# Kernel optimization log

Hardware: AMD Instinct MI355X
Metric: run time of the kernel (lower is better)

Reference implementation:

```python
import jax, jax.numpy as jnp
import numpy as np

POSE_NUM = 8192
EDGE_NUM = 1048576  # n*p = 8192*128
E = EDGE_NUM        # number of gathered edges


def setup_inputs() -> dict:
    key = jax.random.key(0)
    k1, k2, k3, k4, k5, k6 = jax.random.split(key, 6)
    # poses: [1, POSE_NUM, 7] = (tx,ty,tz, qx,qy,qz,qw) with unit quaternion (pypose SE3 convention)
    t = jax.random.normal(k1, (1, POSE_NUM, 3), jnp.float32) * 5.0
    q = jax.random.normal(k2, (1, POSE_NUM, 4), jnp.float32)
    q = q / jnp.linalg.norm(q, axis=-1, keepdims=True)
    poses = jnp.concatenate([t, q], axis=-1)
    # patch coords (r, theta): r in [1, 51], theta in [-pi, pi]
    u = jax.random.uniform(k3, (1, EDGE_NUM, 2), jnp.float32)
    r = 1.0 + 50.0 * u[..., 0:1]
    theta = (2.0 * u[..., 1:2] - 1.0) * jnp.float32(np.pi)
    patch_coords = jnp.concatenate([r, theta], axis=-1)
    # elevation angle phi: small angles typical of sonar beams
    elevation_angle = jax.random.normal(k4, (1, EDGE_NUM, 1), jnp.float32) * 0.3
    # target coords (in init_ba these come from a transform + delta; random is math-equivalent for the residual)
    target_coords = jax.random.normal(k5, (1, E, 2), jnp.float32)
    poses_idx = jax.random.randint(k6, (E,), 0, POSE_NUM, jnp.int32)
    patch_idx = jax.random.randint(jax.random.fold_in(k6, 1), (E,), 0, EDGE_NUM, jnp.int32)
    return {"poses": poses, "patch_coords": patch_coords, "elevation_angle": elevation_angle,
            "target_coords": target_coords, "poses_idx": poses_idx, "patch_idx": patch_idx}


def reference(poses, patch_coords, elevation_angle, target_coords, poses_idx, patch_idx):
    # --- gather per-edge data ---
    p = poses[0, poses_idx]                    # [E, 7]
    rt = patch_coords[0, patch_idx]            # [E, 2] (r, theta)
    phi = elevation_angle[0, patch_idx, 0]     # [E]
    r, theta = rt[:, 0], rt[:, 1]
    # --- polar -> cartesian (spherical sonar convention) ---
    cphi = jnp.cos(phi)
    pts = jnp.stack([r * cphi * jnp.cos(theta),
                     r * cphi * jnp.sin(theta),
                     r * jnp.sin(phi)], axis=-1)        # [E, 3]
    # --- SE3 action: R(q) @ pts + t, q = (qx,qy,qz,qw) unit quaternion ---
    t, qv, qw = p[:, :3], p[:, 3:6], p[:, 6:7]
    uv = jnp.cross(qv, pts)
    pts_w = pts + 2.0 * (qw * uv + jnp.cross(qv, uv)) + t  # [E, 3]
    # --- cartesian -> polar; residual only needs (r, theta) ---
    x, y, z = pts_w[:, 0], pts_w[:, 1], pts_w[:, 2]
    r_out = jnp.sqrt(x * x + y * y + z * z)
    theta_out = jnp.arctan2(y, x)
    proj = jnp.stack([r_out, theta_out], axis=-1)[None]   # [1, E, 2]
    return proj - target_coords
```

## Files before the change

### kernel.cpp

```cpp
#include <hip/hip_runtime.h>
#include <math.h>


#define EDGE_COUNT 1048576

__global__ __launch_bounds__(256) void ba_edge_kernel(
    const float*  __restrict__ poses,
    const float2* __restrict__ patch_coords,
    const float*  __restrict__ elev,
    const float2* __restrict__ target,
    const int*    __restrict__ poses_idx,
    const int*    __restrict__ patch_idx,
    float2*       __restrict__ out,
    int n)
{
    int e = blockIdx.x * blockDim.x + threadIdx.x;
    if (e >= n) return;

    const int pi = poses_idx[e];
    const int ki = patch_idx[e];

    const float2 rt  = patch_coords[ki];
    const float  phi = elev[ki];
    const float  r = rt.x, theta = rt.y;

    float sphi, cphi, st, ct;
    __sincosf(phi,   &sphi, &cphi);
    __sincosf(theta, &st,   &ct);

    const float rc = r * cphi;
    const float px = rc * ct;
    const float py = rc * st;
    const float pz = r * sphi;

    const float* p = poses + pi * 7;
    const float tx = p[0], ty = p[1], tz = p[2];
    const float qx = p[3], qy = p[4], qz = p[5], qw = p[6];

    const float ux = qy * pz - qz * py;
    const float uy = qz * px - qx * pz;
    const float uz = qx * py - qy * px;
    const float cx = qy * uz - qz * uy;
    const float cy = qz * ux - qx * uz;
    const float cz = qx * uy - qy * ux;

    const float x = px + 2.0f * (qw * ux + cx) + tx;
    const float y = py + 2.0f * (qw * uy + cy) + ty;
    const float z = pz + 2.0f * (qw * uz + cz) + tz;

    const float r_out     = sqrtf(x * x + y * y + z * z);
    const float theta_out = atan2f(y, x);

    const float2 tg = target[e];
    out[e] = make_float2(r_out - tg.x, theta_out - tg.y);
}

extern "C" void kernel_launch(void* const* d_in, const int* in_sizes, int n_in,
                              void* d_out, int out_size, void* d_ws, size_t ws_size,
                              hipStream_t stream) {
    const float*  poses        = (const float*)d_in[0];
    const float2* patch_coords = (const float2*)d_in[1];
    const float*  elev         = (const float*)d_in[2];
    const float2* target       = (const float2*)d_in[3];
    const int*    poses_idx    = (const int*)d_in[4];
    const int*    patch_idx    = (const int*)d_in[5];

    const int n = in_sizes[4];
    float2* out = (float2*)d_out;

    const int block = 256;
    const int grid  = (n + block - 1) / block;
    ba_edge_kernel<<<grid, block, 0, stream>>>(
        poses, patch_coords, elev, target, poses_idx, patch_idx, out, n);
}
```

Measured before the change: 34.82 us.

## Repack poses to aligned float4 pairs, process two edges per thread, fast atan2

A small pre-kernel writes each 7-float pose into the workspace as two aligned float4s, so the per-edge pose gather becomes two vector loads instead of seven scalar loads. The main kernel handles two edges per thread, using int2/float4 loads for the indices and targets and a single float4 store. atan2f is replaced by a polynomial approximation built on the hardware reciprocal. The extra launch adds fixed overhead, and the approximation slightly changes accuracy.

```diff
diff --git a/kernel.cpp b/kernel.cpp
--- a/kernel.cpp
+++ b/kernel.cpp
@@ -2,24 +2,38 @@
 #include <math.h>
 
 
-#define EDGE_COUNT 1048576
+#define POSE_NUM 8192
 
-__global__ __launch_bounds__(256) void ba_edge_kernel(
-    const float*  __restrict__ poses,
+__global__ __launch_bounds__(256) void repack_poses_kernel(
+    const float* __restrict__ poses,
+    float4* __restrict__ pose8)
+{
+    int i = blockIdx.x * blockDim.x + threadIdx.x;
+    if (i >= POSE_NUM) return;
+    const float* p = poses + i * 7;
+    pose8[i * 2 + 0] = make_float4(p[0], p[1], p[2], p[3]);
+    pose8[i * 2 + 1] = make_float4(p[4], p[5], p[6], 0.0f);
+}
+
+__device__ __forceinline__ float fast_atan2f(float y, float x) {
+    float ax = fabsf(x), ay = fabsf(y);
+    float mx = fmaxf(ax, ay), mn = fminf(ax, ay);
+    float t = mn * __builtin_amdgcn_rcpf(fmaxf(mx, 1e-30f));
+    float s = t * t;
+    float r = fmaf(s, fmaf(s, fmaf(s, fmaf(s, 0.0208351f, -0.0851330f),
+                                   0.1801410f), -0.3302995f), 0.9998660f) * t;
+    if (ay > ax) r = 1.5707963267948966f - r;
+    if (x < 0.0f) r = 3.14159265358979f - r;
+    return y < 0.0f ? -r : r;
+}
+
+__device__ __forceinline__ void edge_compute(
+    int pi, int ki,
     const float2* __restrict__ patch_coords,
     const float*  __restrict__ elev,
-    const float2* __restrict__ target,
-    const int*    __restrict__ poses_idx,
-    const int*    __restrict__ patch_idx,
-    float2*       __restrict__ out,
-    int n)
+    const float4* __restrict__ pose8,
+    float tgx, float tgy, float* ox, float* oy)
 {
-    int e = blockIdx.x * blockDim.x + threadIdx.x;
-    if (e >= n) return;
-
-    const int pi = poses_idx[e];
-    const int ki = patch_idx[e];
-
     const float2 rt  = patch_coords[ki];
     const float  phi = elev[ki];
     const float  r = rt.x, theta = rt.y;
@@ -33,9 +47,10 @@
     const float py = rc * st;
     const float pz = r * sphi;
 
-    const float* p = poses + pi * 7;
-    const float tx = p[0], ty = p[1], tz = p[2];
-    const float qx = p[3], qy = p[4], qz = p[5], qw = p[6];
+    const float4 pa = pose8[pi * 2 + 0];
+    const float4 pb = pose8[pi * 2 + 1];
+    const float tx = pa.x, ty = pa.y, tz = pa.z;
+    const float qx = pa.w, qy = pb.x, qz = pb.y, qw = pb.z;
 
     const float ux = qy * pz - qz * py;
     const float uy = qz * px - qx * pz;
@@ -48,11 +63,69 @@
     const float y = py + 2.0f * (qw * uy + cy) + ty;
     const float z = pz + 2.0f * (qw * uz + cz) + tz;
 
-    const float r_out     = sqrtf(x * x + y * y + z * z);
-    const float theta_out = atan2f(y, x);
+    *ox = sqrtf(x * x + y * y + z * z) - tgx;
+    *oy = fast_atan2f(y, x) - tgy;
+}
 
+__global__ __launch_bounds__(256) void ba_edge_kernel2(
+    const float2* __restrict__ patch_coords,
+    const float*  __restrict__ elev,
+    const float2* __restrict__ target,
+    const int*    __restrict__ poses_idx,
+    const int*    __restrict__ patch_idx,
+    const float4* __restrict__ pose8,
+    float4*       __restrict__ out,
+    int half_n)
+{
+    int t = blockIdx.x * blockDim.x + threadIdx.x;
+    if (t >= half_n) return;
+
+    const int2 pidx = ((const int2*)poses_idx)[t];
+    const int2 kidx = ((const int2*)patch_idx)[t];
+    const float4 tg = ((const float4*)target)[t];
+
+    float4 o;
+    edge_compute(pidx.x, kidx.x, patch_coords, elev, pose8, tg.x, tg.y, &o.x, &o.y);
+    edge_compute(pidx.y, kidx.y, patch_coords, elev, pose8, tg.z, tg.w, &o.z, &o.w);
+    out[t] = o;
+}
+
+__global__ __launch_bounds__(256) void ba_edge_kernel1(
+    const float*  __restrict__ poses,
+    const float2* __restrict__ patch_coords,
+    const float*  __restrict__ elev,
+    const float2* __restrict__ target,
+    const int*    __restrict__ poses_idx,
+    const int*    __restrict__ patch_idx,
+    float2*       __restrict__ out,
+    int n)
+{
+    int e = blockIdx.x * blockDim.x + threadIdx.x;
+    if (e >= n) return;
+    const int pi = poses_idx[e];
+    const int ki = patch_idx[e];
+    const float2 rt  = patch_coords[ki];
+    const float  phi = elev[ki];
+    float sphi, cphi, st, ct;
+    __sincosf(phi, &sphi, &cphi);
+    __sincosf(rt.y, &st, &ct);
+    const float rc = rt.x * cphi;
+    const float px = rc * ct, py = rc * st, pz = rt.x * sphi;
+    const float* p = poses + pi * 7;
+    const float tx = p[0], ty = p[1], tz = p[2];
+    const float qx = p[3], qy = p[4], qz = p[5], qw = p[6];
+    const float ux = qy * pz - qz * py;
+    const float uy = qz * px - qx * pz;
+    const float uz = qx * py - qy * px;
+    const float cx = qy * uz - qz * uy;
+    const float cy = qz * ux - qx * uz;
+    const float cz = qx * uy - qy * ux;
+    const float x = px + 2.0f * (qw * ux + cx) + tx;
+    const float y = py + 2.0f * (qw * uy + cy) + ty;
+    const float z = pz + 2.0f * (qw * uz + cz) + tz;
     const float2 tg = target[e];
-    out[e] = make_float2(r_out - tg.x, theta_out - tg.y);
+    out[e] = make_float2(sqrtf(x * x + y * y + z * z) - tg.x,
+                         fast_atan2f(y, x) - tg.y);
 }
 
 extern "C" void kernel_launch(void* const* d_in, const int* in_sizes, int n_in,
@@ -64,12 +137,20 @@
     const float2* target       = (const float2*)d_in[3];
     const int*    poses_idx    = (const int*)d_in[4];
     const int*    patch_idx    = (const int*)d_in[5];
+    const int n = in_sizes[4];
 
-    const int n = in_sizes[4];
-    float2* out = (float2*)d_out;
+    const size_t pose8_bytes = (size_t)POSE_NUM * 8 * sizeof(float);
 
-    const int block = 256;
-    const int grid  = (n + block - 1) / block;
-    ba_edge_kernel<<<grid, block, 0, stream>>>(
-        poses, patch_coords, elev, target, poses_idx, patch_idx, out, n);
+    if (ws_size >= pose8_bytes && (n & 1) == 0) {
+        float4* pose8 = (float4*)d_ws;
+        repack_poses_kernel<<<(POSE_NUM + 255) / 256, 256, 0, stream>>>(poses, pose8);
+        const int half_n = n / 2;
+        ba_edge_kernel2<<<(half_n + 255) / 256, 256, 0, stream>>>(
+            patch_coords, elev, target, poses_idx, patch_idx, pose8,
+            (float4*)d_out, half_n);
+    } else {
+        ba_edge_kernel1<<<(n + 255) / 256, 256, 0, stream>>>(
+            poses, patch_coords, elev, target, poses_idx, patch_idx,
+            (float2*)d_out, n);
+    }
 }
```

Result: slower. 41.37 us (+18.8%).
